# Kernel tuning notes

Hardware: AMD Instinct MI355X
Metric: run time of the kernel (lower is better)

Reference implementation:

```python
import jax, jax.numpy as jnp
import numpy as np


def _lstm(x, Wih, Whh, bih, bhh):
    # x: [T,B,E] -> outputs [T,B,H]; torch gate order i,f,g,o
    B = x.shape[1]
    H = Whh.shape[1]
    bias = bih + bhh
    def step(carry, xt):
        h, c = carry
        g = xt @ Wih.T + h @ Whh.T + bias  # [B,4H]
        i, f, gg, o = jnp.split(g, 4, axis=-1)
        c = jax.nn.sigmoid(f) * c + jax.nn.sigmoid(i) * jnp.tanh(gg)
        h = jax.nn.sigmoid(o) * jnp.tanh(c)
        return (h, c), h
    init = (jnp.zeros((B, H), x.dtype), jnp.zeros((B, H), x.dtype))
    _, hs = jax.lax.scan(step, init, x)
    return hs


def setup_inputs():
    key = jax.random.key(0)
    ks = jax.random.split(key, 16)
    B, T, V, NT, E, H = 128, 512, 50000, 24, 128, 256
    Hd = H // 2  # per-direction hidden
    s = 0.08
    x = jax.random.randint(ks[0], (B, T), 0, V)
    tags = jax.random.randint(ks[1], (B, T), 0, NT)
    lengths = jax.random.randint(ks[2], (B,), T // 2, T + 1)
    mask = jnp.arange(T)[None, :] < lengths[:, None]  # [B,T] bool, position 0 always valid
    emb = (jax.random.normal(ks[3], (V, E)) * s).at[0].set(0.0)  # padding_idx=0 row zeroed
    Wih_f = jax.random.normal(ks[4], (4 * Hd, E)) * s
    Whh_f = jax.random.normal(ks[5], (4 * Hd, Hd)) * s
    bih_f = jax.random.normal(ks[6], (4 * Hd,)) * s
    bhh_f = jax.random.normal(ks[7], (4 * Hd,)) * s
    Wih_b = jax.random.normal(ks[8], (4 * Hd, E)) * s
    Whh_b = jax.random.normal(ks[9], (4 * Hd, Hd)) * s
    bih_b = jax.random.normal(ks[10], (4 * Hd,)) * s
    bhh_b = jax.random.normal(ks[11], (4 * Hd,)) * s
    W_out = jax.random.normal(ks[12], (NT, H)) * s
    b_out = jnp.zeros((NT,))
    transitions = jax.random.normal(ks[13], (NT, NT))
    start_trans = jax.random.normal(ks[14], (NT,))
    end_trans = jax.random.normal(ks[15], (NT,))
    return {"x": x, "tags": tags, "mask": mask, "emb": emb,
            "Wih_f": Wih_f, "Whh_f": Whh_f, "bih_f": bih_f, "bhh_f": bhh_f,
            "Wih_b": Wih_b, "Whh_b": Whh_b, "bih_b": bih_b, "bhh_b": bhh_b,
            "W_out": W_out, "b_out": b_out, "transitions": transitions,
            "start_trans": start_trans, "end_trans": end_trans}


def reference(x, tags, mask, emb, Wih_f, Whh_f, bih_f, bhh_f,
              Wih_b, Whh_b, bih_b, bhh_b, W_out, b_out,
              transitions, start_trans, end_trans):
    # --- emissions (dropout is identity in eval) ---
    xe = emb[x]                       # [B,T,E]
    xt = xe.transpose(1, 0, 2)        # [T,B,E]
    hf = _lstm(xt, Wih_f, Whh_f, bih_f, bhh_f)               # [T,B,Hd]
    hb = _lstm(xt[::-1], Wih_b, Whh_b, bih_b, bhh_b)[::-1]   # [T,B,Hd]
    h = jnp.concatenate([hf, hb], axis=-1).transpose(1, 0, 2)  # [B,T,H]
    emissions = h @ W_out.T + b_out   # [B,T,NT]

    # --- CRF forward algorithm (logZ) via scan over time ---
    score0 = start_trans + emissions[:, 0]  # [B,NT]
    em_rest = emissions[:, 1:].transpose(1, 0, 2)  # [T-1,B,NT]
    m_rest = mask[:, 1:].T                        # [T-1,B]
    def fwd_step(score, inp):
        em_t, m_t = inp
        ns = jax.nn.logsumexp(score[:, :, None] + transitions[None] + em_t[:, None, :], axis=1)
        return jnp.where(m_t[:, None], ns, score), None
    score, _ = jax.lax.scan(fwd_step, score0, (em_rest, m_rest))
    logZ = jax.nn.logsumexp(score + end_trans, axis=1)  # [B]

    # --- gold path score, fully vectorized ---
    mf = mask.astype(emissions.dtype)
    emit = jnp.take_along_axis(emissions, tags[:, :, None], axis=2)[:, :, 0]  # [B,T]
    trans = transitions[tags[:, :-1], tags[:, 1:]]                            # [B,T-1]
    gold = start_trans[tags[:, 0]] + emit[:, 0] + jnp.sum((trans + emit[:, 1:]) * mf[:, 1:], axis=1)
    last_idx = mask.sum(axis=1) - 1
    last_tags = jnp.take_along_axis(tags, last_idx[:, None], axis=1)[:, 0]
    gold = gold + end_trans[last_tags]

    return jnp.mean(logZ - gold)
```

## Files before the change

### kernel.cpp

```cpp
#include <hip/hip_runtime.h>
#include <hip/hip_bf16.h>

typedef unsigned short u16;
typedef unsigned int   u32;
typedef _Float16 half2_t __attribute__((ext_vector_type(2)));
typedef short    bf16x8 __attribute__((ext_vector_type(8)));
typedef float    f32x4  __attribute__((ext_vector_type(4)));
typedef u32      u32x4v __attribute__((ext_vector_type(4)));

#define TT   512

__device__ __forceinline__ float sigf(float x)  { return 1.0f / (1.0f + __expf(-x)); }
__device__ __forceinline__ float tanhf_(float x){ return 1.0f - 2.0f / (__expf(2.0f * x) + 1.0f); }

__device__ __forceinline__ u16 f2bf(float x) {
  __hip_bfloat16 h = __float2bfloat16(x);
  return *reinterpret_cast<u16*>(&h);
}
__device__ __forceinline__ float bf2f(u16 u) { return __uint_as_float(((u32)u) << 16); }
__device__ __forceinline__ u32 pk2(float a, float b) {
  return (u32)f2bf(a) | ((u32)f2bf(b) << 16);
}
__device__ __forceinline__ u16 f2h(float x) {
  _Float16 h = (_Float16)x;
  union { _Float16 f; u16 u; } c; c.f = h; return c.u;
}
__device__ __forceinline__ half2_t u2h2(u32 v) {
  union { u32 u; half2_t h; } c; c.u = v; return c.h;
}

__global__ __launch_bounds__(256) void prep_k(
    const float* __restrict__ Wih_f, const float* __restrict__ Wih_b,
    const float* __restrict__ Whh_f, const float* __restrict__ Whh_b,
    const float* __restrict__ bih_f, const float* __restrict__ bhh_f,
    const float* __restrict__ bih_b, const float* __restrict__ bhh_b,
    const float* __restrict__ W_out,
    u16* __restrict__ Wb, u32* __restrict__ Whh16, float* __restrict__ bias,
    u32* __restrict__ Wout16)
{
  int i = blockIdx.x * 256 + threadIdx.x;
  {
    int n = i >> 7, k = i & 127;
    float v = (n < 512) ? Wih_f[n * 128 + k] : Wih_b[(n - 512) * 128 + k];
    Wb[i] = f2bf(v);
  }
  if (i < 65536) {
    int d = i >> 15, rem = i & 32767, r = rem >> 6, kp = rem & 63;
    const float* W = d ? Whh_b : Whh_f;
    float f0 = W[r * 128 + 2 * kp], f1 = W[r * 128 + 2 * kp + 1];
    Whh16[i] = (u32)f2h(f0) | ((u32)f2h(f1) << 16);
  }
  if (i < 1024) {
    int d = i >> 9, jj = i & 511;
    bias[i] = d ? (bih_b[jj] + bhh_b[jj]) : (bih_f[jj] + bhh_f[jj]);
  }
  if (i < 3072) {
    Wout16[i] = (u32)f2h(W_out[2 * i]) | ((u32)f2h(W_out[2 * i + 1]) << 16);
  }
}

__global__ __launch_bounds__(256) void embed_k(
    const int* __restrict__ x, const float* __restrict__ emb, u16* __restrict__ xe)
{
  const int tid = threadIdx.x;
  const int r = blockIdx.x * 8 + (tid >> 5);
  const int lane = tid & 31;
  int token = x[r];
  float4 v = *(const float4*)&emb[(size_t)token * 128 + lane * 4];
  uint2 p; p.x = pk2(v.x, v.y); p.y = pk2(v.z, v.w);
  *(uint2*)&xe[(size_t)r * 128 + lane * 4] = p;
}

__global__ __launch_bounds__(256, 2) void gates_mfma_k(
    const u16* __restrict__ xe, const u16* __restrict__ Wb,
    const float* __restrict__ bias, u16* __restrict__ Gout)
{
  const int tid = threadIdx.x;
  const int wid = tid >> 6, l = tid & 63;
  const int wm = wid >> 1, wn = wid & 1;
  const int M0 = blockIdx.y * 128, N0 = blockIdx.x * 128;
  const int lr = l & 15, lk = l >> 4;

  f32x4 acc[4][4];
#pragma unroll
  for (int i = 0; i < 4; ++i)
#pragma unroll
    for (int j = 0; j < 4; ++j) acc[i][j] = (f32x4){0.f, 0.f, 0.f, 0.f};

#pragma unroll
  for (int ks = 0; ks < 4; ++ks) {
    bf16x8 a[4], b[4];
#pragma unroll
    for (int mi = 0; mi < 4; ++mi)
      a[mi] = *(const bf16x8*)&xe[(size_t)(M0 + wm * 64 + mi * 16 + lr) * 128 + ks * 32 + lk * 8];
#pragma unroll
    for (int ni = 0; ni < 4; ++ni)
      b[ni] = *(const bf16x8*)&Wb[(size_t)(N0 + wn * 64 + ni * 16 + lr) * 128 + ks * 32 + lk * 8];
#pragma unroll
    for (int mi = 0; mi < 4; ++mi)
#pragma unroll
      for (int ni = 0; ni < 4; ++ni)
        acc[mi][ni] = __builtin_amdgcn_mfma_f32_16x16x32_bf16(a[mi], b[ni], acc[mi][ni], 0, 0, 0);
  }

  float bcol[4];
#pragma unroll
  for (int ni = 0; ni < 4; ++ni) bcol[ni] = bias[N0 + wn * 64 + ni * 16 + lr];

  __shared__ u16 cs[128][136];
#pragma unroll
  for (int mi = 0; mi < 4; ++mi)
#pragma unroll
    for (int ni = 0; ni < 4; ++ni) {
      int col = wn * 64 + ni * 16 + lr;
#pragma unroll
      for (int r = 0; r < 4; ++r) {
        int row = wm * 64 + mi * 16 + lk * 4 + r;
        cs[row][col] = f2bf(acc[mi][ni][r] + bcol[ni]);
      }
    }
  __syncthreads();
  {
    int row = tid >> 1, c0 = (tid & 1) * 64;
    u16* dst = &Gout[(size_t)(M0 + row) * 1024 + N0 + c0];
#pragma unroll
    for (int q = 0; q < 8; ++q)
      *(uint4*)&dst[q * 8] = *(const uint4*)&cs[row][c0 + q * 8];
  }
}

__global__ __launch_bounds__(512, 1) void lstm_k(
    const u16* __restrict__ G, const u32* __restrict__ Whh16,
    u16* __restrict__ Hout)
{
  const int bid = blockIdx.x;
  const int dir = bid >> 7, b = bid & 127;
  const int j   = threadIdx.x;
  const int w   = j >> 6, l = j & 63;
  const int u   = 16 * w + (l & 15);
  const int gate = j >> 7;

  const u32* wp = Whh16 + ((size_t)dir << 15) + (size_t)j * 64;
#define LDQ(n) u32x4v q##n = *(const u32x4v*)(wp + 4*(n));
  LDQ(0)  LDQ(1)  LDQ(2)  LDQ(3)  LDQ(4)  LDQ(5)  LDQ(6)  LDQ(7)
  LDQ(8)  LDQ(9)  LDQ(10) LDQ(11) LDQ(12) LDQ(13) LDQ(14) LDQ(15)
#undef LDQ

  __shared__ __align__(16) u32 hs2[64];
  __shared__ float gact[512];
  if (j < 64) hs2[j] = 0u;
  float c = 0.0f;
  __syncthreads();

  const u16* gp = G + (size_t)b * TT * 1024 + (size_t)dir * 512;
  int t = dir ? (TT - 1) : 0;
  const int ts = dir ? -1 : 1;
  u16 cur = gp[(size_t)t * 1024 + j];
  u16 nxt = gp[(size_t)(t + ts) * 1024 + j];

  for (int step = 0; step < TT; ++step) {
    u16 pf = 0;
    if (step + 2 < TT) pf = gp[(size_t)(t + 2 * ts) * 1024 + j];
    float gpre = bf2f(cur);

    float a0 = 0.f, a1 = 0.f;
    const u32x4v* h4 = (const u32x4v*)hs2;
#define DOT(n) { u32x4v hv = h4[n]; \
    a0 = __builtin_amdgcn_fdot2(u2h2(hv.x), u2h2(q##n.x), a0, false); \
    a0 = __builtin_amdgcn_fdot2(u2h2(hv.y), u2h2(q##n.y), a0, false); \
    a1 = __builtin_amdgcn_fdot2(u2h2(hv.z), u2h2(q##n.z), a1, false); \
    a1 = __builtin_amdgcn_fdot2(u2h2(hv.w), u2h2(q##n.w), a1, false); }
    DOT(0)  DOT(1)  DOT(2)  DOT(3)  DOT(4)  DOT(5)  DOT(6)  DOT(7)
    DOT(8)  DOT(9)  DOT(10) DOT(11) DOT(12) DOT(13) DOT(14) DOT(15)
#undef DOT

#define PIN(a,b,c,d) asm volatile("" : "+v"(a), "+v"(b), "+v"(c), "+v"(d));
    PIN(q0,q1,q2,q3)   PIN(q4,q5,q6,q7)   PIN(q8,q9,q10,q11)   PIN(q12,q13,q14,q15)
#undef PIN

    float v = gpre + a0 + a1;
    float a = (gate == 2) ? tanhf_(v) : sigf(v);
    gact[j] = a;
    __syncthreads();
    if ((l & 48) == 0) {
      float iv = gact[u], fv = gact[128 + u], gv = gact[256 + u], ov = gact[384 + u];
      c = fv * c + iv * gv;
      float hvv = ov * tanhf_(c);
      ((u16*)hs2)[u] = f2h(hvv);
      Hout[((size_t)(b * TT + t)) * 256 + dir * 128 + u] = f2h(hvv);
    }
    __syncthreads();
    cur = nxt; nxt = pf;
    t += ts;
  }
}

__global__ __launch_bounds__(256) void emis_k(
    const u16* __restrict__ Hb, const u32* __restrict__ Wout16,
    const float* __restrict__ b_out, float* __restrict__ em)
{
  __shared__ __align__(16) u32 wl2[24 * 128];
  __shared__ float bo[24];
  const int tid = threadIdx.x;
  for (int i = tid; i < 3072; i += 256) wl2[i] = Wout16[i];
  if (tid < 24) bo[tid] = b_out[tid];
  __syncthreads();

  const int m = blockIdx.x * 256 + tid;
  float acc[24];
#pragma unroll
  for (int tg = 0; tg < 24; ++tg) acc[tg] = bo[tg];

  const u32* h2 = (const u32*)(Hb + (size_t)m * 256);
  for (int ck = 0; ck < 16; ++ck) {
    uint4 hv = *(const uint4*)(h2 + ck * 4);
#pragma unroll
    for (int tg = 0; tg < 24; ++tg) {
      u32x4v wv = *(const u32x4v*)&wl2[tg * 128 + ck * 4];
      float a = acc[tg];
      a = __builtin_amdgcn_fdot2(u2h2(hv.x), u2h2(wv.x), a, false);
      a = __builtin_amdgcn_fdot2(u2h2(hv.y), u2h2(wv.y), a, false);
      a = __builtin_amdgcn_fdot2(u2h2(hv.z), u2h2(wv.z), a, false);
      a = __builtin_amdgcn_fdot2(u2h2(hv.w), u2h2(wv.w), a, false);
      acc[tg] = a;
    }
  }
#pragma unroll
  for (int t6 = 0; t6 < 6; ++t6) {
    float4 o;
    o.x = acc[t6*4+0]; o.y = acc[t6*4+1]; o.z = acc[t6*4+2]; o.w = acc[t6*4+3];
    *(float4*)&em[(size_t)m * 24 + t6 * 4] = o;
  }
}

__device__ __forceinline__ int get_mask(const void* mp, int idx, bool byte_mode) {
  return byte_mode ? (int)((const unsigned char*)mp)[idx] : ((const int*)mp)[idx];
}

__global__ __launch_bounds__(64) void crf_k(
    const float* __restrict__ em, const int* __restrict__ tags,
    const void* __restrict__ maskp, const float* __restrict__ trans,
    const float* __restrict__ start_tr, const float* __restrict__ end_tr,
    float* __restrict__ out)
{
  const int b = blockIdx.x;
  const int tid = threadIdx.x;
  const bool byte_mode = (*(const u32*)maskp != 1u);

  int cnt = 0;
  for (int t = tid; t < TT; t += 64) cnt += get_mask(maskp, b * TT + t, byte_mode);
#pragma unroll
  for (int off = 32; off > 0; off >>= 1) cnt += __shfl_down(cnt, off);
  cnt = __shfl(cnt, 0);

  const bool act = (tid < 48);
  const int j  = (tid < 24) ? tid : tid - 24;
  const int i0 = (tid < 24) ? 0 : 12;
  const int partner = (tid < 24) ? tid + 24 : tid - 24;

  float tr_reg[12];
  if (act) {
#pragma unroll
    for (int k = 0; k < 12; ++k) tr_reg[k] = trans[(i0 + k) * 24 + j];
  }

  float sc = 0.f;
  if (act) sc = start_tr[j] + em[(size_t)(b * TT) * 24 + j];
  float em_next = 0.f;
  if (act && cnt > 1) em_next = em[(size_t)(b * TT + 1) * 24 + j];

  for (int t = 1; t < cnt; ++t) {
    float em_cur = em_next;
    if (act && t + 1 < cnt) em_next = em[(size_t)(b * TT + t + 1) * 24 + j];

    float v[12];
#pragma unroll
    for (int k = 0; k < 12; ++k) v[k] = __shfl(sc, i0 + k) + tr_reg[k];
    float mx = fmaxf(fmaxf(fmaxf(v[0], v[1]), fmaxf(v[2], v[3])),
                     fmaxf(fmaxf(v[4], v[5]), fmaxf(v[6], v[7])));
    mx = fmaxf(mx, fmaxf(fmaxf(v[8], v[9]), fmaxf(v[10], v[11])));
    float s = 0.f;
#pragma unroll
    for (int k = 0; k < 12; ++k) s += __expf(v[k] - mx);
    float mo = __shfl(mx, partner), so = __shfl(s, partner);
    float M = fmaxf(mx, mo);
    s = s * __expf(mx - M) + so * __expf(mo - M);
    sc = act ? (em_cur + M + __logf(s)) : 0.f;
  }

  float z = (tid < 24) ? sc + end_tr[tid] : -1e30f;
  float zm = z;
#pragma unroll
  for (int off = 32; off > 0; off >>= 1) zm = fmaxf(zm, __shfl_xor(zm, off));
  float ze = (tid < 24) ? __expf(z - zm) : 0.f;
#pragma unroll
  for (int off = 32; off > 0; off >>= 1) ze += __shfl_xor(ze, off);
  float lzv = zm + __logf(ze);

  float part = 0.f;
  for (int t = tid; t < TT; t += 64) {
    if (t >= 1 && t < cnt) {
      int tp = tags[b * TT + t - 1], tc = tags[b * TT + t];
      part += trans[tp * 24 + tc] + em[((size_t)(b * TT + t)) * 24 + tc];
    }
  }
#pragma unroll
  for (int off = 32; off > 0; off >>= 1) part += __shfl_down(part, off);
  if (tid == 0) {
    int t0g = tags[b * TT];
    float gold = start_tr[t0g] + em[(size_t)(b * TT) * 24 + t0g] + part;
    gold += end_tr[tags[b * TT + cnt - 1]];
    atomicAdd(out, (lzv - gold) * (1.0f / 128.0f));
  }
}

extern "C" void kernel_launch(void* const* d_in, const int* in_sizes, int n_in,
                              void* d_out, int out_size, void* d_ws, size_t ws_size,
                              hipStream_t stream) {
  const int*   x     = (const int*)d_in[0];
  const int*   tags  = (const int*)d_in[1];
  const void*  mask  = d_in[2];
  const float* emb   = (const float*)d_in[3];
  const float* Wih_f = (const float*)d_in[4];
  const float* Whh_f = (const float*)d_in[5];
  const float* bih_f = (const float*)d_in[6];
  const float* bhh_f = (const float*)d_in[7];
  const float* Wih_b = (const float*)d_in[8];
  const float* Whh_b = (const float*)d_in[9];
  const float* bih_b = (const float*)d_in[10];
  const float* bhh_b = (const float*)d_in[11];
  const float* W_out = (const float*)d_in[12];
  const float* b_out = (const float*)d_in[13];
  const float* trans = (const float*)d_in[14];
  const float* st_tr = (const float*)d_in[15];
  const float* en_tr = (const float*)d_in[16];

  u16*   Gb     = (u16*)d_ws;
  u16*   Hb     = Gb + (size_t)65536 * 1024;
  float* em     = (float*)(Hb + (size_t)65536 * 256);
  float* bias   = em + (size_t)65536 * 24;
  u16*   Wb     = (u16*)(bias + 1024);
  u32*   Whh16  = (u32*)(Wb + 131072);
  u32*   Wout16 = Whh16 + 65536;
  u16*   xe     = Hb;

  prep_k<<<512, 256, 0, stream>>>(Wih_f, Wih_b, Whh_f, Whh_b,
                                  bih_f, bhh_f, bih_b, bhh_b, W_out,
                                  Wb, Whh16, bias, Wout16);
  embed_k<<<8192, 256, 0, stream>>>(x, emb, xe);
  gates_mfma_k<<<dim3(8, 512), 256, 0, stream>>>(xe, Wb, bias, Gb);
  lstm_k<<<256, 512, 0, stream>>>(Gb, Whh16, Hb);
  emis_k<<<256, 256, 0, stream>>>(Hb, Wout16, b_out, em);
  hipMemsetAsync(d_out, 0, sizeof(float), stream);
  crf_k<<<128, 64, 0, stream>>>(em, tags, mask, trans, st_tr, en_tr, (float*)d_out);
}
```

Baseline: 694.8 us.

## Batch 16 sequences per block and compute LSTM recurrence with bf16 MFMA

Measured after the change: 1.458 ms. 2.1x slower.

```diff
diff --git a/kernel.cpp b/kernel.cpp
--- a/kernel.cpp
+++ b/kernel.cpp
@@ -35,7 +35,7 @@
     const float* __restrict__ bih_f, const float* __restrict__ bhh_f,
     const float* __restrict__ bih_b, const float* __restrict__ bhh_b,
     const float* __restrict__ W_out,
-    u16* __restrict__ Wb, u32* __restrict__ Whh16, float* __restrict__ bias,
+    u16* __restrict__ Wb, u16* __restrict__ Whhb, float* __restrict__ bias,
     u32* __restrict__ Wout16)
 {
   int i = blockIdx.x * 256 + threadIdx.x;
@@ -44,11 +44,10 @@
     float v = (n < 512) ? Wih_f[n * 128 + k] : Wih_b[(n - 512) * 128 + k];
     Wb[i] = f2bf(v);
   }
-  if (i < 65536) {
-    int d = i >> 15, rem = i & 32767, r = rem >> 6, kp = rem & 63;
+  {
+    int d = i >> 16, rem = i & 65535, n = rem >> 7, k = rem & 127;
     const float* W = d ? Whh_b : Whh_f;
-    float f0 = W[r * 128 + 2 * kp], f1 = W[r * 128 + 2 * kp + 1];
-    Whh16[i] = (u32)f2h(f0) | ((u32)f2h(f1) << 16);
+    Whhb[i] = f2bf(W[n * 128 + k]);
   }
   if (i < 1024) {
     int d = i >> 9, jj = i & 511;
@@ -129,68 +128,101 @@
   }
 }
 
-__global__ __launch_bounds__(512, 1) void lstm_k(
-    const u16* __restrict__ G, const u32* __restrict__ Whh16,
+__global__ __launch_bounds__(512, 1) void lstm_mfma_k(
+    const u16* __restrict__ G, const u16* __restrict__ Whhb,
     u16* __restrict__ Hout)
 {
   const int bid = blockIdx.x;
-  const int dir = bid >> 7, b = bid & 127;
-  const int j   = threadIdx.x;
-  const int w   = j >> 6, l = j & 63;
-  const int u   = 16 * w + (l & 15);
-  const int gate = j >> 7;
-
-  const u32* wp = Whh16 + ((size_t)dir << 15) + (size_t)j * 64;
-#define LDQ(n) u32x4v q##n = *(const u32x4v*)(wp + 4*(n));
-  LDQ(0)  LDQ(1)  LDQ(2)  LDQ(3)  LDQ(4)  LDQ(5)  LDQ(6)  LDQ(7)
-  LDQ(8)  LDQ(9)  LDQ(10) LDQ(11) LDQ(12) LDQ(13) LDQ(14) LDQ(15)
-#undef LDQ
-
-  __shared__ __align__(16) u32 hs2[64];
-  __shared__ float gact[512];
-  if (j < 64) hs2[j] = 0u;
-  float c = 0.0f;
+  const int dir = bid & 1;
+  const int grp = bid >> 1;
+  const int tid = threadIdx.x;
+  const int w = tid >> 6, l = tid & 63;
+  const int lr = l & 15, lk = l >> 4;
+
+  const u16* wb = Whhb + ((size_t)dir << 16);
+  bf16x8 B[16];
+#pragma unroll
+  for (int nt = 0; nt < 4; ++nt)
+#pragma unroll
+    for (int ks = 0; ks < 4; ++ks)
+      B[nt * 4 + ks] = *(const bf16x8*)&wb[(size_t)(w * 64 + nt * 16 + lr) * 128 + ks * 32 + lk * 8];
+
+  __shared__ u16  hlds[16][136];
+  __shared__ float gact[16][522];
+
+  for (int i = tid; i < 16 * 136; i += 512) ((u16*)hlds)[i] = 0;
+  float cst0 = 0.f, cst1 = 0.f, cst2 = 0.f, cst3 = 0.f;
+
+  const int ts = dir ? -1 : 1;
+  int t = dir ? (TT - 1) : 0;
+  const int bs_base = grp * 16 + lk * 4;
+  const int colg = dir * 512 + w * 64;
+
+  u16 gcur[16], gnxt[16];
+#pragma unroll
+  for (int nt = 0; nt < 4; ++nt)
+#pragma unroll
+    for (int r = 0; r < 4; ++r)
+      gcur[nt * 4 + r] = G[(size_t)((bs_base + r) * 512 + t) * 1024 + colg + nt * 16 + lr];
   __syncthreads();
 
-  const u16* gp = G + (size_t)b * TT * 1024 + (size_t)dir * 512;
-  int t = dir ? (TT - 1) : 0;
-  const int ts = dir ? -1 : 1;
-  u16 cur = gp[(size_t)t * 1024 + j];
-  u16 nxt = gp[(size_t)(t + ts) * 1024 + j];
-
   for (int step = 0; step < TT; ++step) {
-    u16 pf = 0;
-    if (step + 2 < TT) pf = gp[(size_t)(t + 2 * ts) * 1024 + j];
-    float gpre = bf2f(cur);
-
-    float a0 = 0.f, a1 = 0.f;
-    const u32x4v* h4 = (const u32x4v*)hs2;
-#define DOT(n) { u32x4v hv = h4[n]; \
-    a0 = __builtin_amdgcn_fdot2(u2h2(hv.x), u2h2(q##n.x), a0, false); \
-    a0 = __builtin_amdgcn_fdot2(u2h2(hv.y), u2h2(q##n.y), a0, false); \
-    a1 = __builtin_amdgcn_fdot2(u2h2(hv.z), u2h2(q##n.z), a1, false); \
-    a1 = __builtin_amdgcn_fdot2(u2h2(hv.w), u2h2(q##n.w), a1, false); }
-    DOT(0)  DOT(1)  DOT(2)  DOT(3)  DOT(4)  DOT(5)  DOT(6)  DOT(7)
-    DOT(8)  DOT(9)  DOT(10) DOT(11) DOT(12) DOT(13) DOT(14) DOT(15)
-#undef DOT
+    if (step + 1 < TT) {
+#pragma unroll
+      for (int nt = 0; nt < 4; ++nt)
+#pragma unroll
+        for (int r = 0; r < 4; ++r)
+          gnxt[nt * 4 + r] = G[(size_t)((bs_base + r) * 512 + (t + ts)) * 1024 + colg + nt * 16 + lr];
+    }
+
+    bf16x8 A[4];
+#pragma unroll
+    for (int ks = 0; ks < 4; ++ks)
+      A[ks] = *(const bf16x8*)&hlds[lr][ks * 32 + lk * 8];
+
+    f32x4 acc[4];
+#pragma unroll
+    for (int nt = 0; nt < 4; ++nt) acc[nt] = (f32x4){0.f, 0.f, 0.f, 0.f};
+#pragma unroll
+    for (int ks = 0; ks < 4; ++ks)
+#pragma unroll
+      for (int nt = 0; nt < 4; ++nt)
+        acc[nt] = __builtin_amdgcn_mfma_f32_16x16x32_bf16(A[ks], B[nt * 4 + ks], acc[nt], 0, 0, 0);
 
 #define PIN(a,b,c,d) asm volatile("" : "+v"(a), "+v"(b), "+v"(c), "+v"(d));
-    PIN(q0,q1,q2,q3)   PIN(q4,q5,q6,q7)   PIN(q8,q9,q10,q11)   PIN(q12,q13,q14,q15)
+    PIN(B[0], B[1], B[2], B[3])   PIN(B[4], B[5], B[6], B[7])
+    PIN(B[8], B[9], B[10], B[11]) PIN(B[12], B[13], B[14], B[15])
 #undef PIN
 
-    float v = gpre + a0 + a1;
-    float a = (gate == 2) ? tanhf_(v) : sigf(v);
-    gact[j] = a;
+#pragma unroll
+    for (int nt = 0; nt < 4; ++nt) {
+      const int n = w * 64 + nt * 16 + lr;
+      const int gate = n >> 7;
+#pragma unroll
+      for (int r = 0; r < 4; ++r) {
+        float g = acc[nt][r] + bf2f(gcur[nt * 4 + r]);
+        float a = (gate == 2) ? tanhf_(g) : sigf(g);
+        gact[lk * 4 + r][n] = a;
+      }
+    }
     __syncthreads();
-    if ((l & 48) == 0) {
-      float iv = gact[u], fv = gact[128 + u], gv = gact[256 + u], ov = gact[384 + u];
-      c = fv * c + iv * gv;
-      float hvv = ov * tanhf_(c);
-      ((u16*)hs2)[u] = f2h(hvv);
-      Hout[((size_t)(b * TT + t)) * 256 + dir * 128 + u] = f2h(hvv);
+
+#pragma unroll
+    for (int r = 0; r < 4; ++r) {
+      int idx = tid + r * 512;
+      int s = idx >> 7, u = idx & 127;
+      float iv = gact[s][u], fv = gact[s][128 + u], gv = gact[s][256 + u], ov = gact[s][384 + u];
+      float cv = (r == 0) ? cst0 : (r == 1) ? cst1 : (r == 2) ? cst2 : cst3;
+      cv = fv * cv + iv * gv;
+      float hv = ov * tanhf_(cv);
+      if (r == 0) cst0 = cv; else if (r == 1) cst1 = cv; else if (r == 2) cst2 = cv; else cst3 = cv;
+      hlds[s][u] = f2bf(hv);
+      Hout[(size_t)((grp * 16 + s) * 512 + t) * 256 + dir * 128 + u] = f2h(hv);
     }
     __syncthreads();
-    cur = nxt; nxt = pf;
+
+#pragma unroll
+    for (int i = 0; i < 16; ++i) gcur[i] = gnxt[i];
     t += ts;
   }
 }
@@ -340,16 +372,16 @@
   float* em     = (float*)(Hb + (size_t)65536 * 256);
   float* bias   = em + (size_t)65536 * 24;
   u16*   Wb     = (u16*)(bias + 1024);
-  u32*   Whh16  = (u32*)(Wb + 131072);
-  u32*   Wout16 = Whh16 + 65536;
+  u16*   Whhb   = Wb + 131072;
+  u32*   Wout16 = (u32*)(Whhb + 131072);
   u16*   xe     = Hb;
 
   prep_k<<<512, 256, 0, stream>>>(Wih_f, Wih_b, Whh_f, Whh_b,
                                   bih_f, bhh_f, bih_b, bhh_b, W_out,
-                                  Wb, Whh16, bias, Wout16);
+                                  Wb, Whhb, bias, Wout16);
   embed_k<<<8192, 256, 0, stream>>>(x, emb, xe);
   gates_mfma_k<<<dim3(8, 512), 256, 0, stream>>>(xe, Wb, bias, Gb);
-  lstm_k<<<256, 512, 0, stream>>>(Gb, Whh16, Hb);
+  lstm_mfma_k<<<16, 512, 0, stream>>>(Gb, Whhb, Hb);
   emis_k<<<256, 256, 0, stream>>>(Hb, Wout16, b_out, em);
   hipMemsetAsync(d_out, 0, sizeof(float), stream);
   crf_k<<<128, 64, 0, stream>>>(em, tags, mask, trans, st_tr, en_tr, (float*)d_out);
```
